# Performance work log

Measured on AMD Instinct MI355X. Metric: run time of the kernel, lower is better.

## Reference

```python
import jax, jax.numpy as jnp
import numpy as np

N_SRC, N_DST, E = 50000, 50000, 800000
D_GT, D_AG = 64, 64
HID, HEADS = 256, 4
FPH = HID // HEADS  # 64
N_ACT = 16
NEG_SLOPE = 0.2  # DGL GATv2Conv default negative_slope


def setup_inputs() -> dict:
    key = jax.random.key(0)
    ks = jax.random.split(key, 16)
    f32 = jnp.float32
    return {
        "feat_gt": jax.random.normal(ks[0], (N_SRC, D_GT), f32),
        "feat_agent": jax.random.normal(ks[1], (N_DST, D_AG), f32),
        "h0": jax.random.normal(ks[2], (N_DST, HID), f32),
        "edge_src": jax.random.randint(ks[3], (E,), 0, N_SRC),
        "edge_dst": jax.random.randint(ks[4], (E,), 0, N_DST),
        "W_src": jax.random.normal(ks[5], (D_GT, HID), f32) * 0.1,
        "b_src": jnp.zeros((HID,), f32),
        "W_dst": jax.random.normal(ks[6], (D_AG, HID), f32) * 0.1,
        "b_dst": jnp.zeros((HID,), f32),
        "attn": jax.random.normal(ks[7], (HEADS, FPH), f32) * 0.1,
        "W_res": jax.random.normal(ks[8], (D_AG, HID), f32) * 0.1,
        "b_res": jnp.zeros((HID,), f32),
        "W_ih": jax.random.normal(ks[9], (3 * HID, HID), f32) * 0.05,
        "W_hh": jax.random.normal(ks[10], (3 * HID, HID), f32) * 0.05,
        "b_ih": jnp.zeros((3 * HID,), f32),
        "b_hh": jnp.zeros((3 * HID,), f32),
        "W_out": jax.random.normal(ks[11], (HID, N_ACT), f32) * 0.05,
        "b_out": jnp.zeros((N_ACT,), f32),
    }


def _gatv2(feat_gt, feat_agent, edge_src, edge_dst,
           W_src, b_src, W_dst, b_dst, attn, W_res, b_res):
    # GATv2Conv (bipartite, share_weights=False, residual=True, activation=ReLU)
    fs = (feat_gt @ W_src + b_src).reshape(N_SRC, HEADS, FPH)    # [Ns,H,F]
    fd = (feat_agent @ W_dst + b_dst).reshape(N_DST, HEADS, FPH)  # [Nd,H,F]
    e = fs[edge_src] + fd[edge_dst]                               # [E,H,F]
    e = jnp.where(e > 0, e, NEG_SLOPE * e)                        # LeakyReLU
    score = jnp.einsum('ehf,hf->eh', e, attn)                     # [E,H]
    # edge softmax segmented by destination node
    smax = jax.lax.stop_gradient(
        jax.ops.segment_max(score, edge_dst, num_segments=N_DST))  # [Nd,H]
    ex = jnp.exp(score - smax[edge_dst])
    den = jax.ops.segment_sum(ex, edge_dst, num_segments=N_DST)   # [Nd,H]
    alpha = ex / den[edge_dst]                                    # [E,H]
    msg = alpha[:, :, None] * fs[edge_src]                        # [E,H,F]
    rst = jax.ops.segment_sum(msg, edge_dst, num_segments=N_DST)  # [Nd,H,F]
    rst = rst.reshape(N_DST, HID) + (feat_agent @ W_res + b_res)  # residual
    return jax.nn.relu(rst)


def _gru_cell(x, h, W_ih, W_hh, b_ih, b_hh):
    gi = x @ W_ih.T + b_ih
    gh = h @ W_hh.T + b_hh
    ir, iz, inn = jnp.split(gi, 3, axis=-1)
    hr, hz, hn = jnp.split(gh, 3, axis=-1)
    r = jax.nn.sigmoid(ir + hr)
    z = jax.nn.sigmoid(iz + hz)
    n = jnp.tanh(inn + r * hn)
    return (1.0 - z) * n + z * h


def reference(feat_gt, feat_agent, h0, edge_src, edge_dst,
              W_src, b_src, W_dst, b_dst, attn, W_res, b_res,
              W_ih, W_hh, b_ih, b_hh, W_out, b_out):
    x = _gatv2(feat_gt, feat_agent, edge_src, edge_dst,
               W_src, b_src, W_dst, b_dst, attn, W_res, b_res)  # [Nd,HID]
    h = _gru_cell(x, h0, W_ih, W_hh, b_ih, b_hh)                # [Nd,HID]
    logits = h @ W_out + b_out                                  # [Nd,N_ACT]
    return (logits, h)
```

## Files before the change

kernel.cpp:

```cpp
#include <hip/hip_runtime.h>
#include <stdint.h>

#define N_SRCN 50000
#define N_DSTN 50000
#define NE     800000
#define HIDN   256
#define NEG    0.2f

typedef __attribute__((ext_vector_type(8)))  short short8;
typedef __attribute__((ext_vector_type(16))) float float16v;

__device__ __forceinline__ float bf2f(unsigned short u){
    union { unsigned u32; float f; } c; c.u32 = ((unsigned)u) << 16; return c.f;
}
__device__ __forceinline__ unsigned short f2bf(float f){
    union { float f; unsigned u; } c; c.f = f;
    unsigned r = c.u + 0x7fffu + ((c.u >> 16) & 1u);
    return (unsigned short)(r >> 16);
}
__device__ __forceinline__ float4 ld4b(const unsigned short* p){
    uint2 u = *reinterpret_cast<const uint2*>(p);
    float4 r;
    r.x = bf2f((unsigned short)(u.x & 0xffff));
    r.y = bf2f((unsigned short)(u.x >> 16));
    r.z = bf2f((unsigned short)(u.y & 0xffff));
    r.w = bf2f((unsigned short)(u.y >> 16));
    return r;
}
__device__ __forceinline__ void gload_lds16(const unsigned short* g, unsigned short* l){
    __builtin_amdgcn_global_load_lds(
        (const __attribute__((address_space(1))) void*)g,
        (__attribute__((address_space(3))) void*)l,
        16, 0, 0);
}

__global__ void pack_kernel(const float* __restrict__ Wsrc, const float* __restrict__ Wdst,
                            const float* __restrict__ Wres, const float* __restrict__ Wih,
                            const float* __restrict__ Whh,
                            unsigned short* __restrict__ Wt2,
                            unsigned short* __restrict__ Wf){
    int i = blockIdx.x * 256 + threadIdx.x;
    if (i < 49152){
        int which = i >> 14, j = i & 16383;
        int k = j >> 8, c = j & 255;
        const float* W = (which == 0) ? Wsrc : (which == 1 ? Wdst : Wres);
        float v = W[j];
        int off = which * 16384 + (c >> 5) * 2048 + (k >> 4) * 512
                + (((k >> 3) & 1) * 32 + (c & 31)) * 8 + (k & 7);
        Wt2[off] = f2bf(v);
    } else if (i < 49152 + 196608){
        int o = i - 49152;
        int row = o >> 8, k = o & 255;
        int g = row >> 8, c = row & 255;
        float v = Wih[o];
        int off = g * 131072 + (c >> 5) * 16384 + (k >> 4) * 512
                + (((k >> 3) & 1) * 32 + (c & 31)) * 8 + (k & 7);
        Wf[off] = f2bf(v);
    } else if (i < 49152 + 393216){
        int o = i - 49152 - 196608;
        int row = o >> 8, k = o & 255;
        int g = row >> 8, c = row & 255;
        float v = Whh[o];
        int off = g * 131072 + (c >> 5) * 16384 + (16 + (k >> 4)) * 512
                + (((k >> 3) & 1) * 32 + (c & 31)) * 8 + (k & 7);
        Wf[off] = f2bf(v);
    }
}

__global__ __launch_bounds__(256) void proj_kernel(
        const float* __restrict__ Agt, const float* __restrict__ Aag,
        const unsigned short* __restrict__ Wt2,
        const float* __restrict__ bsrc, const float* __restrict__ bdst,
        const float* __restrict__ bres,
        unsigned short* __restrict__ fs, unsigned short* __restrict__ fd,
        unsigned short* __restrict__ resb){
    __shared__ unsigned short As[64 * 72];
    __shared__ unsigned short Cs[64 * 72];
    int z = blockIdx.z;
    const float* A = (z == 0) ? Agt : Aag;
    const float* bias = (z == 0) ? bsrc : (z == 1 ? bdst : bres);
    unsigned short* out = (z == 0) ? fs : (z == 1 ? fd : resb);
    const unsigned short* Wb = Wt2 + z * 16384;
    int tid = threadIdx.x;
    int m0 = blockIdx.y * 64;
    #pragma unroll
    for (int i = 0; i < 4; ++i){
        int ci = tid + i * 256;
        int row = ci >> 4;
        int k4 = (ci & 15) << 2;
        int gr = m0 + row; if (gr >= N_SRCN) gr = N_SRCN - 1;
        float4 v = *reinterpret_cast<const float4*>(A + (size_t)gr * 64 + k4);
        unsigned short* dp = As + row * 72 + k4;
        dp[0] = f2bf(v.x); dp[1] = f2bf(v.y); dp[2] = f2bf(v.z); dp[3] = f2bf(v.w);
    }
    __syncthreads();
    int lane = tid & 63, w = tid >> 6;
    int l31 = lane & 31, half = lane >> 5;
    int msub = (w & 1) * 32;
    int cbw = blockIdx.x * 2 + (w >> 1);
    const unsigned short* bb = Wb + cbw * 2048 + lane * 8;
    const unsigned short* ap = As + (msub + l31) * 72 + half * 8;
    float16v acc = {0,0,0,0,0,0,0,0,0,0,0,0,0,0,0,0};
    #pragma unroll
    for (int ks = 0; ks < 4; ++ks){
        short8 a = *reinterpret_cast<const short8*>(ap + ks * 16);
        short8 b = *reinterpret_cast<const short8*>(bb + ks * 512);
        acc = __builtin_amdgcn_mfma_f32_32x32x16_bf16(a, b, acc, 0, 0, 0);
    }
    float bv = bias[cbw * 32 + l31];
    int ccol = (w >> 1) * 32 + l31;
    #pragma unroll
    for (int r = 0; r < 16; ++r){
        int row = (r & 3) + 8 * (r >> 2) + 4 * half + msub;
        Cs[row * 72 + ccol] = f2bf(acc[r] + bv);
    }
    __syncthreads();
    int srow = tid >> 2, chunk = tid & 3;
    int gr2 = m0 + srow;
    if (gr2 < N_SRCN){
        const uint4* sp = reinterpret_cast<const uint4*>(Cs + srow * 72 + chunk * 16);
        uint4* gp = reinterpret_cast<uint4*>(out + (size_t)gr2 * 256 + blockIdx.x * 64 + chunk * 16);
        gp[0] = sp[0];
        gp[1] = sp[1];
    }
}

__global__ void degree_kernel(const int* __restrict__ dst, int* __restrict__ deg){
    int i = blockIdx.x * 256 + threadIdx.x;
    if (i < NE) atomicAdd(&deg[dst[i]], 1);
}

__global__ void scan1_kernel(const int* __restrict__ deg, int* __restrict__ bsum){
    __shared__ int s[256];
    int tid = threadIdx.x;
    int i = blockIdx.x * 256 + tid;
    s[tid] = (i < N_DSTN) ? deg[i] : 0;
    __syncthreads();
    #pragma unroll
    for (int off = 128; off; off >>= 1){
        if (tid < off) s[tid] += s[tid + off];
        __syncthreads();
    }
    if (tid == 0) bsum[blockIdx.x] = s[0];
}

__global__ void scan2_kernel(const int* __restrict__ bsum, int* __restrict__ boff){
    __shared__ int s[256];
    int tid = threadIdx.x;
    int v = (tid < 196) ? bsum[tid] : 0;
    s[tid] = v;
    __syncthreads();
    #pragma unroll
    for (int off = 1; off < 256; off <<= 1){
        int t = (tid >= off) ? s[tid - off] : 0;
        __syncthreads();
        s[tid] += t;
        __syncthreads();
    }
    if (tid < 196) boff[tid] = s[tid] - v;
}

__global__ void scan3_kernel(const int* __restrict__ deg, const int* __restrict__ boff,
                             int* __restrict__ ptr, int* __restrict__ cursor){
    __shared__ int s[256];
    int tid = threadIdx.x;
    int i = blockIdx.x * 256 + tid;
    int v = (i < N_DSTN) ? deg[i] : 0;
    s[tid] = v;
    __syncthreads();
    #pragma unroll
    for (int off = 1; off < 256; off <<= 1){
        int t = (tid >= off) ? s[tid - off] : 0;
        __syncthreads();
        s[tid] += t;
        __syncthreads();
    }
    int ex = s[tid] - v + boff[blockIdx.x];
    if (i < N_DSTN){ ptr[i] = ex; cursor[i] = ex; }
}

__global__ void scatter_kernel(const int* __restrict__ src, const int* __restrict__ dst,
                               int* __restrict__ cursor, int* __restrict__ csr){
    int i = blockIdx.x * 256 + threadIdx.x;
    if (i < NE){
        int d = dst[i];
        int pos = atomicAdd(&cursor[d], 1);
        csr[pos] = src[i];
    }
}

__global__ __launch_bounds__(256) void aggregate_kernel(
        const unsigned short* __restrict__ fs, const unsigned short* __restrict__ fd,
        const unsigned short* __restrict__ res, const float* __restrict__ attn,
        const int* __restrict__ ptr, const int* __restrict__ deg,
        const int* __restrict__ csr, unsigned short* __restrict__ x){
    int wv = threadIdx.x >> 6;
    int d = blockIdx.x * 4 + wv;
    if (d >= N_DSTN) return;
    int lane = threadIdx.x & 63;
    int c4 = lane * 4;
    float4 fdv = ld4b(fd + (size_t)d * 256 + c4);
    float4 at = *reinterpret_cast<const float4*>(attn + (lane >> 4) * 64 + (lane & 15) * 4);
    int p = ptr[d], dg = deg[d];
    float l = 0.f;
    float4 acc = make_float4(0.f, 0.f, 0.f, 0.f);
    for (int base = 0; base < dg; base += 64){
        int cnt = min(64, dg - base);
        int sreg = (lane < cnt) ? csr[p + base + lane] : 0;
        float4 b0 = ld4b(fs + (size_t)__shfl(sreg, 0) * 256 + c4);
        float4 b1 = ld4b(fs + (size_t)__shfl(sreg, 1 & 63) * 256 + c4);
        float4 b2 = ld4b(fs + (size_t)__shfl(sreg, 2 & 63) * 256 + c4);
        float4 b3 = ld4b(fs + (size_t)__shfl(sreg, 3 & 63) * 256 + c4);
        for (int j = 0; j < cnt; j += 4){
            float4 n0 = ld4b(fs + (size_t)__shfl(sreg, (j + 4) & 63) * 256 + c4);
            float4 n1 = ld4b(fs + (size_t)__shfl(sreg, (j + 5) & 63) * 256 + c4);
            float4 n2 = ld4b(fs + (size_t)__shfl(sreg, (j + 6) & 63) * 256 + c4);
            float4 n3 = ld4b(fs + (size_t)__shfl(sreg, (j + 7) & 63) * 256 + c4);
#define PROC(BV, T) { \
            float ex = BV.x + fdv.x; ex = ex > 0.f ? ex : NEG * ex; \
            float ey = BV.y + fdv.y; ey = ey > 0.f ? ey : NEG * ey; \
            float ez = BV.z + fdv.z; ez = ez > 0.f ? ez : NEG * ez; \
            float ew = BV.w + fdv.w; ew = ew > 0.f ? ew : NEG * ew; \
            float part = ex * at.x + ey * at.y + ez * at.z + ew * at.w; \
            part += __shfl_xor(part, 1); \
            part += __shfl_xor(part, 2); \
            part += __shfl_xor(part, 4); \
            part += __shfl_xor(part, 8); \
            float wgt = ((j + (T)) < cnt) ? __expf(part) : 0.f; \
            l += wgt; \
            acc.x = fmaf(wgt, BV.x, acc.x); \
            acc.y = fmaf(wgt, BV.y, acc.y); \
            acc.z = fmaf(wgt, BV.z, acc.z); \
            acc.w = fmaf(wgt, BV.w, acc.w); }
            PROC(b0, 0) PROC(b1, 1) PROC(b2, 2) PROC(b3, 3)
#undef PROC
            b0 = n0; b1 = n1; b2 = n2; b3 = n3;
        }
    }
    float inv = (l > 0.f) ? 1.f / l : 0.f;
    float4 rv = ld4b(res + (size_t)d * 256 + c4);
    float xx = fmaxf(fmaf(acc.x, inv, rv.x), 0.f);
    float xy = fmaxf(fmaf(acc.y, inv, rv.y), 0.f);
    float xz = fmaxf(fmaf(acc.z, inv, rv.z), 0.f);
    float xw = fmaxf(fmaf(acc.w, inv, rv.w), 0.f);
    uint2 o;
    o.x = (unsigned)f2bf(xx) | ((unsigned)f2bf(xy) << 16);
    o.y = (unsigned)f2bf(xz) | ((unsigned)f2bf(xw) << 16);
    *reinterpret_cast<uint2*>(x + (size_t)d * 256 + c4) = o;
}

__global__ __launch_bounds__(512, 4) void gru_kernel(
        const unsigned short* __restrict__ Xb,
        const float* __restrict__ H0, const unsigned short* __restrict__ Wf,
        const float* __restrict__ bih, const float* __restrict__ bhh,
        float* __restrict__ outH){
    __shared__ unsigned short As[2 * 32 * 256];
    __shared__ unsigned short Bs[2 * 12288];
    int tid = threadIdx.x;
    int m0 = blockIdx.x << 5;
    int w = tid >> 6, lane = tid & 63;

    #pragma unroll
    for (int i = 0; i < 2; ++i){
        int g = w + i * 8;
        int row = 2 * g + (lane >> 5);
        int gr = m0 + row; if (gr >= N_DSTN) gr = N_DSTN - 1;
        int j = lane & 31;
        const unsigned short* src = Xb + (size_t)gr * 256 + ((j ^ (row & 15)) << 3);
        gload_lds16(src, As + g * 512);
    }
    int s0 = 3 * w, s1 = 3 * w + 1, s2 = 3 * w + 2;
    const unsigned short* g0 = Wf + (s0 >> 3) * 131072 + (s0 & 7) * 16384 + lane * 8;
    const unsigned short* g1 = Wf + (s1 >> 3) * 131072 + (s1 & 7) * 16384 + lane * 8;
    const unsigned short* g2 = Wf + (s2 >> 3) * 131072 + (s2 & 7) * 16384 + lane * 8;
    gload_lds16(g0, Bs + s0 * 512);
    gload_lds16(g1, Bs + s1 * 512);
    gload_lds16(g2, Bs + s2 * 512);
    {
        int hrow = tid >> 4, hseg = tid & 15;
        int hgr = m0 + hrow; if (hgr >= N_DSTN) hgr = N_DSTN - 1;
        const float* hp = H0 + (size_t)hgr * 256 + hseg * 16;
        float4 f0 = *reinterpret_cast<const float4*>(hp);
        float4 f1 = *reinterpret_cast<const float4*>(hp + 4);
        float4 f2 = *reinterpret_cast<const float4*>(hp + 8);
        float4 f3 = *reinterpret_cast<const float4*>(hp + 12);
        int rl = hrow & 15;
        int c0 = hseg * 2;
        uint4 o;
        o.x = (unsigned)f2bf(f0.x) | ((unsigned)f2bf(f0.y) << 16);
        o.y = (unsigned)f2bf(f0.z) | ((unsigned)f2bf(f0.w) << 16);
        o.z = (unsigned)f2bf(f1.x) | ((unsigned)f2bf(f1.y) << 16);
        o.w = (unsigned)f2bf(f1.z) | ((unsigned)f2bf(f1.w) << 16);
        *reinterpret_cast<uint4*>(As + 8192 + hrow * 256 + ((c0 ^ rl) << 3)) = o;
        o.x = (unsigned)f2bf(f2.x) | ((unsigned)f2bf(f2.y) << 16);
        o.y = (unsigned)f2bf(f2.z) | ((unsigned)f2bf(f2.w) << 16);
        o.z = (unsigned)f2bf(f3.x) | ((unsigned)f2bf(f3.y) << 16);
        o.w = (unsigned)f2bf(f3.z) | ((unsigned)f2bf(f3.w) << 16);
        *reinterpret_cast<uint4*>(As + 8192 + hrow * 256 + (((c0 + 1) ^ rl) << 3)) = o;
    }
    asm volatile("s_waitcnt vmcnt(0) lgkmcnt(0)" ::: "memory");
    __syncthreads();

    int l31 = lane & 31, half = lane >> 5;
    int ct = w;
    int arow = l31;
    int rl = arow & 15;
    float16v zv = {0,0,0,0,0,0,0,0,0,0,0,0,0,0,0,0};
    float16v ar = zv, az = zv, anx = zv, anh = zv;
    #pragma unroll
    for (int p = 0; p < 32; ++p){
        asm volatile("s_waitcnt vmcnt(0)" ::: "memory");
        __builtin_amdgcn_s_barrier();
        __builtin_amdgcn_sched_barrier(0);
        if (p + 1 < 32){
            unsigned short* db = Bs + ((p + 1) & 1) * 12288;
            gload_lds16(g0 + (p + 1) * 512, db + s0 * 512);
            gload_lds16(g1 + (p + 1) * 512, db + s1 * 512);
            gload_lds16(g2 + (p + 1) * 512, db + s2 * 512);
        }
        const unsigned short* bp = Bs + (p & 1) * 12288;
        const unsigned short* ap_ = (p < 16) ? As : (As + 8192);
        int kl = p & 15;
        short8 a  = *reinterpret_cast<const short8*>(
                        ap_ + arow * 256 + (((kl * 2 + half) ^ rl) << 3));
        short8 vr = *reinterpret_cast<const short8*>(bp + (0 * 8 + ct) * 512 + lane * 8);
        short8 vz = *reinterpret_cast<const short8*>(bp + (1 * 8 + ct) * 512 + lane * 8);
        short8 vn = *reinterpret_cast<const short8*>(bp + (2 * 8 + ct) * 512 + lane * 8);
        __builtin_amdgcn_s_setprio(1);
        ar = __builtin_amdgcn_mfma_f32_32x32x16_bf16(a, vr, ar, 0, 0, 0);
        az = __builtin_amdgcn_mfma_f32_32x32x16_bf16(a, vz, az, 0, 0, 0);
        if (p < 16) anx = __builtin_amdgcn_mfma_f32_32x32x16_bf16(a, vn, anx, 0, 0, 0);
        else        anh = __builtin_amdgcn_mfma_f32_32x32x16_bf16(a, vn, anh, 0, 0, 0);
        __builtin_amdgcn_s_setprio(0);
    }
    int cg = ct * 32 + l31;
    float rb = bih[cg] + bhh[cg];
    float zb = bih[256 + cg] + bhh[256 + cg];
    float bin = bih[512 + cg], bhn = bhh[512 + cg];
    #pragma unroll
    for (int r = 0; r < 16; ++r){
        int m = m0 + (r & 3) + 8 * (r >> 2) + 4 * half;
        if (m < N_DSTN){
            float h0v = H0[(size_t)m * 256 + cg];
            float rrg = 1.f / (1.f + __expf(-(ar[r] + rb)));
            float zg  = 1.f / (1.f + __expf(-(az[r] + zb)));
            float nx = anx[r] + bin + rrg * (anh[r] + bhn);
            float tm = __expf(-2.f * fabsf(nx));
            float nn = (1.f - tm) / (1.f + tm);
            nn = (nx >= 0.f) ? nn : -nn;
            outH[(size_t)m * 256 + cg] = (1.f - zg) * nn + zg * h0v;
        }
    }
}

__global__ __launch_bounds__(256) void logits_kernel(
        const float* __restrict__ H, const float* __restrict__ Wout,
        const float* __restrict__ bout, float* __restrict__ outL){
    __shared__ float Hl[16 * 260];
    __shared__ float Wl[16 * 260];
    int tid = threadIdx.x;
    int m0 = blockIdx.x * 16;
    #pragma unroll
    for (int i = 0; i < 4; ++i){
        int ci = tid + i * 256;
        int row = ci >> 6;
        int c4 = (ci & 63) << 2;
        int gr = m0 + row; if (gr >= N_DSTN) gr = N_DSTN - 1;
        float4 v = *reinterpret_cast<const float4*>(H + (size_t)gr * 256 + c4);
        float* dp = Hl + row * 260 + c4;
        dp[0] = v.x; dp[1] = v.y; dp[2] = v.z; dp[3] = v.w;
    }
    #pragma unroll
    for (int i = 0; i < 16; ++i){
        int ci = tid + i * 256;
        int c = ci >> 4, j = ci & 15;
        Wl[j * 260 + c] = Wout[c * 16 + j];
    }
    __syncthreads();
    int row = tid >> 4, j = tid & 15;
    const float* hr = Hl + row * 260;
    const float* wr = Wl + j * 260;
    float acc = bout[j];
    #pragma unroll
    for (int c = 0; c < 256; c += 4){
        float4 hv = *reinterpret_cast<const float4*>(hr + c);
        float4 wv = *reinterpret_cast<const float4*>(wr + c);
        acc = fmaf(hv.x, wv.x, fmaf(hv.y, wv.y, fmaf(hv.z, wv.z, fmaf(hv.w, wv.w, acc))));
    }
    int m = m0 + row;
    if (m < N_DSTN) outL[m * 16 + j] = acc;
}

extern "C" void kernel_launch(void* const* d_in, const int* in_sizes, int n_in,
                              void* d_out, int out_size, void* d_ws, size_t ws_size,
                              hipStream_t stream){
    const float* feat_gt = (const float*)d_in[0];
    const float* feat_ag = (const float*)d_in[1];
    const float* h0      = (const float*)d_in[2];
    const int*   e_src   = (const int*)d_in[3];
    const int*   e_dst   = (const int*)d_in[4];
    const float* W_src   = (const float*)d_in[5];
    const float* b_src   = (const float*)d_in[6];
    const float* W_dst   = (const float*)d_in[7];
    const float* b_dst   = (const float*)d_in[8];
    const float* attn    = (const float*)d_in[9];
    const float* W_res   = (const float*)d_in[10];
    const float* b_res   = (const float*)d_in[11];
    const float* W_ih    = (const float*)d_in[12];
    const float* W_hh    = (const float*)d_in[13];
    const float* b_ih    = (const float*)d_in[14];
    const float* b_hh    = (const float*)d_in[15];
    const float* W_out   = (const float*)d_in[16];
    const float* b_out   = (const float*)d_in[17];

    float* outL = (float*)d_out;
    float* outH = outL + (size_t)N_DSTN * 16;

    char* ws = (char*)d_ws;
    size_t off = 0;
    auto alloc = [&](size_t bytes) -> void* {
        void* p = ws + off; off = (off + bytes + 255) & ~(size_t)255; return p;
    };
    unsigned short* fs   = (unsigned short*)alloc((size_t)N_SRCN * 256 * 2);
    unsigned short* fd   = (unsigned short*)alloc((size_t)N_DSTN * 256 * 2);
    unsigned short* res  = (unsigned short*)alloc((size_t)N_DSTN * 256 * 2);
    unsigned short* xb   = (unsigned short*)alloc((size_t)N_DSTN * 256 * 2);
    unsigned short* Wt2  = (unsigned short*)alloc(49152 * 2);
    unsigned short* Wf   = (unsigned short*)alloc(393216 * 2);
    int* deg    = (int*)alloc(N_DSTN * 4);
    int* ptr    = (int*)alloc(N_DSTN * 4);
    int* cursor = (int*)alloc(N_DSTN * 4);
    int* csr    = (int*)alloc((size_t)NE * 4);
    int* bsum   = (int*)alloc(256 * 4);
    int* boff   = (int*)alloc(256 * 4);

    hipMemsetAsync(deg, 0, N_DSTN * 4, stream);
    pack_kernel<<<1728, 256, 0, stream>>>(W_src, W_dst, W_res, W_ih, W_hh, Wt2, Wf);

    proj_kernel<<<dim3(4, 782, 3), 256, 0, stream>>>(feat_gt, feat_ag, Wt2,
                                                     b_src, b_dst, b_res, fs, fd, res);

    degree_kernel<<<3125, 256, 0, stream>>>(e_dst, deg);
    scan1_kernel<<<196, 256, 0, stream>>>(deg, bsum);
    scan2_kernel<<<1, 256, 0, stream>>>(bsum, boff);
    scan3_kernel<<<196, 256, 0, stream>>>(deg, boff, ptr, cursor);
    scatter_kernel<<<3125, 256, 0, stream>>>(e_src, e_dst, cursor, csr);
    aggregate_kernel<<<12500, 256, 0, stream>>>(fs, fd, res, attn, ptr, deg, csr, xb);

    gru_kernel<<<1563, 512, 0, stream>>>(xb, h0, Wf, b_ih, b_hh, outH);
    logits_kernel<<<3125, 256, 0, stream>>>(outH, W_out, b_out, outL);
}
```

Baseline: 456.8 us.

## Load GRU weight fragments directly from global memory instead of LDS staging

The fused GRU weight buffer is repacked so each wave's column tile is contiguous across k-steps, with the r/z/n gates interleaved per k-step. The GRU kernel drops its double-buffered LDS staging of weights, along with the per-iteration barriers, async copies and priority hints. Each wave now reads its MFMA B operands straight from global memory, relying on L2/L1 caching since every block reads the same weights. This removes barrier synchronisation and LDS traffic, but each load now pays global latency with no explicit prefetch.

```diff
diff --git a/kernel.cpp b/kernel.cpp
--- a/kernel.cpp
+++ b/kernel.cpp
@@ -53,7 +53,7 @@
         int row = o >> 8, k = o & 255;
         int g = row >> 8, c = row & 255;
         float v = Wih[o];
-        int off = g * 131072 + (c >> 5) * 16384 + (k >> 4) * 512
+        int off = (c >> 5) * 49152 + (k >> 4) * 1536 + g * 512
                 + (((k >> 3) & 1) * 32 + (c & 31)) * 8 + (k & 7);
         Wf[off] = f2bf(v);
     } else if (i < 49152 + 393216){
@@ -61,7 +61,7 @@
         int row = o >> 8, k = o & 255;
         int g = row >> 8, c = row & 255;
         float v = Whh[o];
-        int off = g * 131072 + (c >> 5) * 16384 + (16 + (k >> 4)) * 512
+        int off = (c >> 5) * 49152 + (16 + (k >> 4)) * 1536 + g * 512
                 + (((k >> 3) & 1) * 32 + (c & 31)) * 8 + (k & 7);
         Wf[off] = f2bf(v);
     }
@@ -255,7 +255,6 @@
         const float* __restrict__ bih, const float* __restrict__ bhh,
         float* __restrict__ outH){
     __shared__ unsigned short As[2 * 32 * 256];
-    __shared__ unsigned short Bs[2 * 12288];
     int tid = threadIdx.x;
     int m0 = blockIdx.x << 5;
     int w = tid >> 6, lane = tid & 63;
@@ -269,13 +268,6 @@
         const unsigned short* src = Xb + (size_t)gr * 256 + ((j ^ (row & 15)) << 3);
         gload_lds16(src, As + g * 512);
     }
-    int s0 = 3 * w, s1 = 3 * w + 1, s2 = 3 * w + 2;
-    const unsigned short* g0 = Wf + (s0 >> 3) * 131072 + (s0 & 7) * 16384 + lane * 8;
-    const unsigned short* g1 = Wf + (s1 >> 3) * 131072 + (s1 & 7) * 16384 + lane * 8;
-    const unsigned short* g2 = Wf + (s2 >> 3) * 131072 + (s2 & 7) * 16384 + lane * 8;
-    gload_lds16(g0, Bs + s0 * 512);
-    gload_lds16(g1, Bs + s1 * 512);
-    gload_lds16(g2, Bs + s2 * 512);
     {
         int hrow = tid >> 4, hseg = tid & 15;
         int hgr = m0 + hrow; if (hgr >= N_DSTN) hgr = N_DSTN - 1;
@@ -303,35 +295,24 @@
 
     int l31 = lane & 31, half = lane >> 5;
     int ct = w;
-    int arow = l31;
-    int rl = arow & 15;
+    int rl = l31 & 15;
+    const unsigned short* bb = Wf + ct * 49152 + lane * 8;
     float16v zv = {0,0,0,0,0,0,0,0,0,0,0,0,0,0,0,0};
     float16v ar = zv, az = zv, anx = zv, anh = zv;
     #pragma unroll
     for (int p = 0; p < 32; ++p){
-        asm volatile("s_waitcnt vmcnt(0)" ::: "memory");
-        __builtin_amdgcn_s_barrier();
-        __builtin_amdgcn_sched_barrier(0);
-        if (p + 1 < 32){
-            unsigned short* db = Bs + ((p + 1) & 1) * 12288;
-            gload_lds16(g0 + (p + 1) * 512, db + s0 * 512);
-            gload_lds16(g1 + (p + 1) * 512, db + s1 * 512);
-            gload_lds16(g2 + (p + 1) * 512, db + s2 * 512);
-        }
-        const unsigned short* bp = Bs + (p & 1) * 12288;
+        const unsigned short* bp = bb + p * 1536;
+        short8 vr = *reinterpret_cast<const short8*>(bp);
+        short8 vz = *reinterpret_cast<const short8*>(bp + 512);
+        short8 vn = *reinterpret_cast<const short8*>(bp + 1024);
         const unsigned short* ap_ = (p < 16) ? As : (As + 8192);
         int kl = p & 15;
-        short8 a  = *reinterpret_cast<const short8*>(
-                        ap_ + arow * 256 + (((kl * 2 + half) ^ rl) << 3));
-        short8 vr = *reinterpret_cast<const short8*>(bp + (0 * 8 + ct) * 512 + lane * 8);
-        short8 vz = *reinterpret_cast<const short8*>(bp + (1 * 8 + ct) * 512 + lane * 8);
-        short8 vn = *reinterpret_cast<const short8*>(bp + (2 * 8 + ct) * 512 + lane * 8);
-        __builtin_amdgcn_s_setprio(1);
+        short8 a = *reinterpret_cast<const short8*>(
+                       ap_ + l31 * 256 + (((kl * 2 + half) ^ rl) << 3));
         ar = __builtin_amdgcn_mfma_f32_32x32x16_bf16(a, vr, ar, 0, 0, 0);
         az = __builtin_amdgcn_mfma_f32_32x32x16_bf16(a, vz, az, 0, 0, 0);
         if (p < 16) anx = __builtin_amdgcn_mfma_f32_32x32x16_bf16(a, vn, anx, 0, 0, 0);
         else        anh = __builtin_amdgcn_mfma_f32_32x32x16_bf16(a, vn, anh, 0, 0, 0);
-        __builtin_amdgcn_s_setprio(0);
     }
     int cg = ct * 32 + l31;
     float rb = bih[cg] + bhh[cg];
```

After: 446.7 us. 2.2% less time.
